# Performance work log

Hardware: AMD Instinct MI355X
Metric: run time of the kernel (lower is better)

Reference implementation:

```python
import jax, jax.numpy as jnp
import numpy as np

EPS = 1e-12  # torch F.normalize default eps
K, C = 64, 128  # num_clusters, dim


def _l2norm(v, axis):
    n = jnp.sqrt(jnp.sum(v * v, axis=axis, keepdims=True))
    return v / jnp.maximum(n, EPS)


def setup_inputs() -> dict:
    key = jax.random.key(0)
    k1, k2, k3, k4 = jax.random.split(key, 4)
    x = jax.random.normal(k1, (32, C, 64, 64), dtype=jnp.float32)
    centroids = jax.random.uniform(k2, (K, C), dtype=jnp.float32)
    # conv weight/bias initialized from centroids like _init_params (alpha=100)
    alpha = 100.0
    conv_w = 2.0 * alpha * centroids                     # [K, C] (1x1 conv)
    conv_b = -alpha * jnp.linalg.norm(centroids, axis=1) # [K]
    return {"x": x, "conv_w": conv_w, "conv_b": conv_b, "centroids": centroids}


def reference(x, conv_w, conv_b, centroids):
    N = x.shape[0]
    # descriptor-wise L2 normalization over channel dim
    x = _l2norm(x, axis=1)
    xf = x.reshape(N, C, -1)  # [N, C, P]
    # 1x1 conv == per-location linear: [N, K, P]
    logits = jnp.einsum('kc,ncp->nkp', conv_w, xf) + conv_b[None, :, None]
    soft_assign = jax.nn.softmax(logits, axis=1)  # softmax over clusters
    # vlad[n,k,c] = sum_p a[n,k,p] * (x[n,c,p] - centroids[k,c])
    # algebraic rewrite avoids the O(N*K*C*P) intermediate (same math)
    vlad = jnp.einsum('nkp,ncp->nkc', soft_assign, xf) \
        - soft_assign.sum(axis=2)[:, :, None] * centroids[None]
    vlad = _l2norm(vlad, axis=2)            # intra-normalization over C
    vlad = vlad.reshape(N, -1)              # [N, K*C]
    vlad = _l2norm(vlad, axis=1)            # global L2 norm
    return vlad
```

## Files before the change

kernel.cpp:

```cpp
#include <hip/hip_runtime.h>

typedef __attribute__((ext_vector_type(4))) float f4;
typedef __attribute__((ext_vector_type(4))) float f32x4;
typedef __attribute__((ext_vector_type(4))) unsigned u32x4;
typedef __attribute__((ext_vector_type(8))) short bf16x8;

#define NK 64
#define NC 128
#define NP 4096
#define NN 32
#define EPSV 1e-12f

#define PCH 64
#define CPB 4
#define NGRPX (NP / (PCH * CPB))

#define WS_WF_SL 0
#define WS_SS    8192
#define WS_VP    (8192 + 32768)
#define WS_SLAB_TOTAL (WS_VP + NGRPX * NN * NK * NC)

#define FB_VLAD 0
#define FB_S    (NN * NK * NC)
#define FB_G    (FB_S + NN * NK)
#define FB_WF   (FB_G + NN)
#define FB_TOTAL (FB_WF + 8192)

__device__ __forceinline__ unsigned short f2bf(float x) {
  unsigned u = __builtin_bit_cast(unsigned, x);
  u += 0x7fffu + ((u >> 16) & 1u);
  return (unsigned short)(u >> 16);
}
__device__ __forceinline__ float bf2f(unsigned short h) {
  unsigned u = ((unsigned)h) << 16;
  return __builtin_bit_cast(float, u);
}
__device__ __forceinline__ unsigned cvtpk(float a, float b) {
  unsigned r;
  asm volatile("v_cvt_pk_bf16_f32 %0, %1, %2" : "=v"(r) : "v"(a), "v"(b));
  return r;
}
__device__ __forceinline__ float asf(unsigned u) { return __builtin_bit_cast(float, u); }

__device__ __forceinline__ void barrier_lds() {
  asm volatile("s_waitcnt lgkmcnt(0)" ::: "memory");
  __builtin_amdgcn_s_barrier();
  asm volatile("" ::: "memory");
  __builtin_amdgcn_sched_barrier(0);
}

__global__ void nv_zero(float* __restrict__ ws) {
  int i = blockIdx.x * blockDim.x + threadIdx.x;
  int stride = gridDim.x * blockDim.x;
  for (; i < FB_WF; i += stride) ws[i] = 0.0f;
}

__global__ void nv_wfrag(const float* __restrict__ conv_w, unsigned short* __restrict__ wfrag) {
  int idx = blockIdx.x * 256 + threadIdx.x;
  if (idx >= 2048) return;
  int lane = idx & 63, hl = (idx >> 6) & 1, ct = (idx >> 7) & 3, kt = idx >> 9;
  int r = lane & 15, g = lane >> 4;
  const float* src = conv_w + (16 * kt + r) * NC + 32 * ct + 8 * g;
  unsigned short o[8];
#pragma unroll
  for (int j = 0; j < 8; ++j) {
    float v = src[j];
    unsigned short h = f2bf(v);
    o[j] = hl ? f2bf(v - bf2f(h)) : h;
  }
  u32x4 pk;
#pragma unroll
  for (int m = 0; m < 4; ++m) pk[m] = (unsigned)o[2 * m] | ((unsigned)o[2 * m + 1] << 16);
  *reinterpret_cast<u32x4*>(wfrag + (size_t)idx * 8) = pk;
}

template <bool SLAB>
__global__ __launch_bounds__(512, 2)
void nv_main(const float* __restrict__ x, const unsigned short* __restrict__ wfrag,
             const float* __restrict__ conv_b, float* __restrict__ vout,
             float* __restrict__ sout) {
  __shared__ __align__(16) unsigned xhl_t[PCH][132];
  __shared__ __align__(16) unsigned short xh[NC][72];
  __shared__ __align__(16) unsigned short a_lds[NK][72];
  __shared__ __align__(16) unsigned short wf_lds[1024][8];
  __shared__ __align__(16) float inv_lds[PCH];
  __shared__ __align__(16) float mx_buf[2][PCH];
  __shared__ __align__(16) float sum_buf[2][PCH];

  const int tid = threadIdx.x;
  const int lane = tid & 63;
  const int w = tid >> 6;
  const int r = lane & 15;
  const int g = lane >> 4;
  const int n = blockIdx.y;
  const int p0loc = (w & 3) << 4;
  const int kp = w >> 2;
  const int ktg0 = kp << 1;
  const int kw = w & 3;
  const int ph = w >> 2;

  for (int s = tid; s < 1024; s += 512) {
    int gs = ((s >> 6) * 2) * 64 + (s & 63);
    *reinterpret_cast<u32x4*>(&wf_lds[s][0]) =
        *reinterpret_cast<const u32x4*>(wfrag + (size_t)gs * 8);
  }
  bf16x8 wlo_r[2][4];
#pragma unroll
  for (int kt2 = 0; kt2 < 2; ++kt2)
#pragma unroll
    for (int ct = 0; ct < 4; ++ct)
      wlo_r[kt2][ct] = *reinterpret_cast<const bf16x8*>(
          wfrag + ((size_t)(((ktg0 + kt2) * 4 + ct) * 2 + 1) * 64 + lane) * 8);
  float bb[2];
#pragma unroll
  for (int kt2 = 0; kt2 < 2; ++kt2) bb[kt2] = conv_b[16 * (ktg0 + kt2) + r];

  f32x4 vacc[8];
#pragma unroll
  for (int t = 0; t < 8; ++t) vacc[t] = (f32x4){0.f, 0.f, 0.f, 0.f};
  float s_part[2] = {0.f, 0.f};

  const int cst = tid & 127;
  const int pq = tid >> 7;
  const int swst = ((cst >> 3) & 3) << 3;
  const int pbase = blockIdx.x * (CPB * PCH);
  const float* xrow = x + ((size_t)n * NC + cst) * NP + 16 * pq;

  f4 pre[4];
#pragma unroll
  for (int q4 = 0; q4 < 4; ++q4)
    pre[q4] = *reinterpret_cast<const f4*>(xrow + pbase + 4 * q4);

  for (int cc = 0; cc < CPB; ++cc) {
#pragma unroll
    for (int q4 = 0; q4 < 4; ++q4) {
      f4 v = pre[q4];
      const int pl = 16 * pq + 4 * q4;
      unsigned h01 = cvtpk(v[0], v[1]);
      unsigned h23 = cvtpk(v[2], v[3]);
      float r0 = v[0] - asf(h01 << 16);
      float r1 = v[1] - asf(h01 & 0xffff0000u);
      float r2 = v[2] - asf(h23 << 16);
      float r3 = v[3] - asf(h23 & 0xffff0000u);
      unsigned l01 = cvtpk(r0, r1);
      unsigned l23 = cvtpk(r2, r3);
      const int pp = pl ^ swst;
      *reinterpret_cast<unsigned*>(&xh[cst][pp]) = h01;
      *reinterpret_cast<unsigned*>(&xh[cst][pp + 2]) = h23;
      xhl_t[pl + 0][cst] = __builtin_amdgcn_perm(h01, l01, 0x05040100u);
      xhl_t[pl + 1][cst] = __builtin_amdgcn_perm(h01, l01, 0x07060302u);
      xhl_t[pl + 2][cst] = __builtin_amdgcn_perm(h23, l23, 0x05040100u);
      xhl_t[pl + 3][cst] = __builtin_amdgcn_perm(h23, l23, 0x07060302u);
    }
    barrier_lds();
    if (cc + 1 < CPB) {
      const float* xb = xrow + pbase + (cc + 1) * PCH;
#pragma unroll
      for (int q4 = 0; q4 < 4; ++q4)
        pre[q4] = *reinterpret_cast<const f4*>(xb + 4 * q4);
    }
    f32x4 d1 = {0.f, 0.f, 0.f, 0.f}, d2 = {0.f, 0.f, 0.f, 0.f};
    f32x4 lac[2];
    lac[0] = (f32x4){0.f, 0.f, 0.f, 0.f};
    lac[1] = (f32x4){0.f, 0.f, 0.f, 0.f};
#pragma unroll
    for (int ct = 0; ct < 4; ++ct) {
      const unsigned* row = &xhl_t[p0loc + r][32 * ct + 8 * g];
      u32x4 wA = *reinterpret_cast<const u32x4*>(row);
      u32x4 wB = *reinterpret_cast<const u32x4*>(row + 4);
      unsigned wv8[8] = {wA[0], wA[1], wA[2], wA[3], wB[0], wB[1], wB[2], wB[3]};
      u32x4 hh, ll;
#pragma unroll
      for (int m = 0; m < 4; ++m) {
        hh[m] = __builtin_amdgcn_perm(wv8[2 * m + 1], wv8[2 * m], 0x07060302u);
        ll[m] = __builtin_amdgcn_perm(wv8[2 * m + 1], wv8[2 * m], 0x05040100u);
      }
      bf16x8 Ah = __builtin_bit_cast(bf16x8, hh);
      bf16x8 Al = __builtin_bit_cast(bf16x8, ll);
      d1 = __builtin_amdgcn_mfma_f32_16x16x32_bf16(Ah, Ah, d1, 0, 0, 0);
      d2 = __builtin_amdgcn_mfma_f32_16x16x32_bf16(Ah, Al, d2, 0, 0, 0);
#pragma unroll
      for (int kt2 = 0; kt2 < 2; ++kt2) {
        const int kt4ct = (ktg0 + kt2) * 4 + ct;
        bf16x8 whi = *reinterpret_cast<const bf16x8*>(&wf_lds[kt4ct * 64 + lane][0]);
        lac[kt2] = __builtin_amdgcn_mfma_f32_16x16x32_bf16(Ah, whi, lac[kt2], 0, 0, 0);
        lac[kt2] = __builtin_amdgcn_mfma_f32_16x16x32_bf16(Al, whi, lac[kt2], 0, 0, 0);
        lac[kt2] = __builtin_amdgcn_mfma_f32_16x16x32_bf16(Ah, wlo_r[kt2][ct], lac[kt2], 0, 0, 0);
      }
    }
    if ((r >> 2) == g) {
      int i = r & 3;
      float nsq = d1[i] + 2.0f * d2[i];
      inv_lds[p0loc + r] = 1.0f / fmaxf(sqrtf(nsq), EPSV);
    }
    asm volatile("s_waitcnt lgkmcnt(0)" ::: "memory");
    __builtin_amdgcn_sched_barrier(0);
    f4 ivv = *reinterpret_cast<const f4*>(&inv_lds[p0loc + 4 * g]);
    float lt[2][4], e[2][4], mpart[4], sp[4];
#pragma unroll
    for (int kt2 = 0; kt2 < 2; ++kt2)
#pragma unroll
      for (int i = 0; i < 4; ++i) lt[kt2][i] = lac[kt2][i] * ivv[i] + bb[kt2];
#pragma unroll
    for (int i = 0; i < 4; ++i) mpart[i] = fmaxf(lt[0][i], lt[1][i]);
#pragma unroll
    for (int o = 1; o <= 8; o <<= 1)
#pragma unroll
      for (int i = 0; i < 4; ++i) mpart[i] = fmaxf(mpart[i], __shfl_xor(mpart[i], o));
#pragma unroll
    for (int i = 0; i < 4; ++i) sp[i] = 0.f;
#pragma unroll
    for (int kt2 = 0; kt2 < 2; ++kt2)
#pragma unroll
      for (int i = 0; i < 4; ++i) {
        e[kt2][i] = __expf(lt[kt2][i] - mpart[i]);
        sp[i] += e[kt2][i];
      }
#pragma unroll
    for (int o = 1; o <= 8; o <<= 1)
#pragma unroll
      for (int i = 0; i < 4; ++i) sp[i] += __shfl_xor(sp[i], o);
    if (r < 4) mx_buf[kp][p0loc + 4 * g + r] = mpart[r];
    else if (r < 8) sum_buf[kp][p0loc + 4 * g + (r - 4)] = sp[r - 4];
    barrier_lds();
    {
      f4 m0 = *reinterpret_cast<const f4*>(&mx_buf[0][p0loc + 4 * g]);
      f4 m1 = *reinterpret_cast<const f4*>(&mx_buf[1][p0loc + 4 * g]);
      f4 s0 = *reinterpret_cast<const f4*>(&sum_buf[0][p0loc + 4 * g]);
      f4 s1 = *reinterpret_cast<const f4*>(&sum_buf[1][p0loc + 4 * g]);
      float fcorr[4];
#pragma unroll
      for (int i = 0; i < 4; ++i) {
        float m = fmaxf(m0[i], m1[i]);
        float c0 = __expf(m0[i] - m);
        float c1 = __expf(m1[i] - m);
        float tot = s0[i] * c0 + s1[i] * c1;
        fcorr[i] = (kp == 0 ? c0 : c1) / tot;
      }
#pragma unroll
      for (int kt2 = 0; kt2 < 2; ++kt2) {
        float av[4];
#pragma unroll
        for (int i = 0; i < 4; ++i) {
          float a = e[kt2][i] * fcorr[i];
          s_part[kt2] += a;
          av[i] = a * ivv[i];
        }
        unsigned* arow = reinterpret_cast<unsigned*>(&a_lds[16 * (ktg0 + kt2) + r][p0loc + 4 * g]);
        arow[0] = cvtpk(av[0], av[1]);
        arow[1] = cvtpk(av[2], av[3]);
      }
    }
    barrier_lds();
    {
      bf16x8 af = *reinterpret_cast<const bf16x8*>(&a_lds[16 * kw + r][32 * ph + 8 * g]);
#pragma unroll
      for (int tcl = 0; tcl < 8; ++tcl) {
        const int c = (tcl << 4) + r;
        const int pblk = ((ph << 2) + g) ^ ((c >> 3) & 3);
        bf16x8 bx = *reinterpret_cast<const bf16x8*>(&xh[c][pblk << 3]);
        vacc[tcl] = __builtin_amdgcn_mfma_f32_16x16x32_bf16(af, bx, vacc[tcl], 0, 0, 0);
      }
    }
    barrier_lds();
  }

  float* cbuf = reinterpret_cast<float*>(&xhl_t[0][0]);
  float* s_red = cbuf + 8192;
  if (w < 4) {
#pragma unroll
    for (int tcl = 0; tcl < 8; ++tcl)
#pragma unroll
      for (int i = 0; i < 4; ++i)
        cbuf[kw * 2048 + (4 * g + i) * 128 + (tcl << 4) + r] = vacc[tcl][i];
  }
#pragma unroll
  for (int kt2 = 0; kt2 < 2; ++kt2) {
    float v = s_part[kt2];
    v += __shfl_xor(v, 16);
    v += __shfl_xor(v, 32);
    if (g == 0) s_red[(kp * 4 + (w & 3)) * 32 + kt2 * 16 + r] = v;
  }
  barrier_lds();
  if (w >= 4) {
#pragma unroll
    for (int tcl = 0; tcl < 8; ++tcl)
#pragma unroll
      for (int i = 0; i < 4; ++i) {
        const int idx = kw * 2048 + (4 * g + i) * 128 + (tcl << 4) + r;
        float v = vacc[tcl][i] + cbuf[idx];
        if constexpr (SLAB) cbuf[idx] = v;
        else atomicAdd(&vout[((size_t)n * NK + 16 * kw + 4 * g + i) * NC + (tcl << 4) + r], v);
      }
  }
  if (tid < 64) {
    float S = 0.f;
#pragma unroll
    for (int pt = 0; pt < 4; ++pt) S += s_red[((tid >> 5) * 4 + pt) * 32 + (tid & 31)];
    if constexpr (SLAB) sout[((size_t)blockIdx.x * NN + n) * NK + tid] = S;
    else atomicAdd(&sout[n * NK + tid], S);
  }
  if constexpr (SLAB) {
    barrier_lds();
    float* dst = vout + ((size_t)blockIdx.x * NN + n) * (NK * NC);
#pragma unroll
    for (int m = 0; m < 4; ++m) {
      const int idx = m * 512 + tid;
      *reinterpret_cast<f4*>(dst + 4 * idx) = *reinterpret_cast<const f4*>(cbuf + 4 * idx);
    }
  }
}

template <bool SLAB>
__global__ void nv_finalize(const float* __restrict__ vin, const float* __restrict__ sin,
                            const float* __restrict__ centroids,
                            float* __restrict__ out, float* __restrict__ gnorm) {
  const int k = blockIdx.x;
  const int n = blockIdx.y;
  const int t = threadIdx.x;
  float S, v0, v1;
  if constexpr (SLAB) {
    float sv = (t < 16) ? sin[((size_t)t * NN + n) * NK + k] : 0.f;
#pragma unroll
    for (int o = 1; o <= 8; o <<= 1) sv += __shfl_xor(sv, o);
    S = __shfl(sv, 0);
    v0 = 0.f; v1 = 0.f;
#pragma unroll
    for (int sx = 0; sx < NGRPX; ++sx) {
      const float* vr = vin + ((size_t)sx * NN + n) * (NK * NC) + k * NC;
      v0 += vr[t];
      v1 += vr[t + 64];
    }
  } else {
    S = sin[n * NK + k];
    const size_t base = ((size_t)n * NK + k) * NC;
    v0 = vin[base + t];
    v1 = vin[base + t + 64];
  }
  v0 -= S * centroids[k * NC + t];
  v1 -= S * centroids[k * NC + t + 64];
  float ss = v0 * v0 + v1 * v1;
#pragma unroll
  for (int off = 1; off < 64; off <<= 1) ss += __shfl_xor(ss, off);
  float inv = 1.0f / fmaxf(sqrtf(ss), EPSV);
  const size_t base = ((size_t)n * NK + k) * NC;
  if constexpr (SLAB) {
    out[base + t] = v0 * inv * 0.125f;
    out[base + t + 64] = v1 * inv * 0.125f;
  } else {
    out[base + t] = v0 * inv;
    out[base + t + 64] = v1 * inv;
    if (t == 0) atomicAdd(&gnorm[n], ss * inv * inv);
  }
}

__global__ void nv_scale(float* __restrict__ out, const float* __restrict__ gnorm) {
  int i = blockIdx.x * blockDim.x + threadIdx.x;
  int n = i >> 13;
  out[i] *= 1.0f / fmaxf(sqrtf(gnorm[n]), EPSV);
}

extern "C" void kernel_launch(void* const* d_in, const int* in_sizes, int n_in,
                              void* d_out, int out_size, void* d_ws, size_t ws_size,
                              hipStream_t stream) {
  const float* x = (const float*)d_in[0];
  const float* conv_w = (const float*)d_in[1];
  const float* conv_b = (const float*)d_in[2];
  const float* centroids = (const float*)d_in[3];
  float* out = (float*)d_out;
  float* ws = (float*)d_ws;

  if (ws_size >= (size_t)WS_SLAB_TOTAL * sizeof(float)) {
    unsigned short* wfrag = (unsigned short*)(ws + WS_WF_SL);
    float* sp = ws + WS_SS;
    float* vp = ws + WS_VP;
    nv_wfrag<<<8, 256, 0, stream>>>(conv_w, wfrag);
    nv_main<true><<<dim3(NGRPX, NN), 512, 0, stream>>>(x, wfrag, conv_b, vp, sp);
    nv_finalize<true><<<dim3(NK, NN), 64, 0, stream>>>(vp, sp, centroids, out, nullptr);
  } else {
    float* vlad_acc = ws + FB_VLAD;
    float* s_acc = ws + FB_S;
    float* gnorm = ws + FB_G;
    unsigned short* wfrag = (unsigned short*)(ws + FB_WF);
    nv_zero<<<256, 256, 0, stream>>>(ws);
    nv_wfrag<<<8, 256, 0, stream>>>(conv_w, wfrag);
    nv_main<false><<<dim3(NGRPX, NN), 512, 0, stream>>>(x, wfrag, conv_b, vlad_acc, s_acc);
    nv_finalize<false><<<dim3(NK, NN), 64, 0, stream>>>(vlad_acc, s_acc, centroids, out, gnorm);
    nv_scale<<<1024, 256, 0, stream>>>(out, gnorm);
  }
}
```

Baseline: 47.28 us.

## Restructure main loop barriers, shuffle inverse norms, prefetch B fragments, widen finalize

The main loop now stages the next chunk's bf16 split at the end of each iteration instead of the start, which removes one block barrier per chunk. The B fragments for the VLAD MFMA are read from LDS before the softmax barrier. Per-pixel inverse norms are broadcast with wave shuffles instead of an LDS round trip with waitcnt, and s_setprio is raised around the MFMA blocks. The finalize kernel packs four clusters per 256-thread block and uses float2 accesses. The early B-fragment reads cost extra registers, and putting STAGE after the MFMAs depends on the xh and xhl_t reuse being correctly fenced.

```diff
diff --git a/kernel.cpp b/kernel.cpp
--- a/kernel.cpp
+++ b/kernel.cpp
@@ -1,5 +1,6 @@
 #include <hip/hip_runtime.h>
 
+typedef __attribute__((ext_vector_type(2))) float f2;
 typedef __attribute__((ext_vector_type(4))) float f4;
 typedef __attribute__((ext_vector_type(4))) float f32x4;
 typedef __attribute__((ext_vector_type(4))) unsigned u32x4;
@@ -83,7 +84,6 @@
   __shared__ __align__(16) unsigned short xh[NC][72];
   __shared__ __align__(16) unsigned short a_lds[NK][72];
   __shared__ __align__(16) unsigned short wf_lds[1024][8];
-  __shared__ __align__(16) float inv_lds[PCH];
   __shared__ __align__(16) float mx_buf[2][PCH];
   __shared__ __align__(16) float sum_buf[2][PCH];
 
@@ -127,11 +127,7 @@
   const float* xrow = x + ((size_t)n * NC + cst) * NP + 16 * pq;
 
   f4 pre[4];
-#pragma unroll
-  for (int q4 = 0; q4 < 4; ++q4)
-    pre[q4] = *reinterpret_cast<const f4*>(xrow + pbase + 4 * q4);
-
-  for (int cc = 0; cc < CPB; ++cc) {
+  auto STAGE = [&]() {
 #pragma unroll
     for (int q4 = 0; q4 < 4; ++q4) {
       f4 v = pre[q4];
@@ -152,7 +148,15 @@
       xhl_t[pl + 2][cst] = __builtin_amdgcn_perm(h23, l23, 0x05040100u);
       xhl_t[pl + 3][cst] = __builtin_amdgcn_perm(h23, l23, 0x07060302u);
     }
-    barrier_lds();
+  };
+
+#pragma unroll
+  for (int q4 = 0; q4 < 4; ++q4)
+    pre[q4] = *reinterpret_cast<const f4*>(xrow + pbase + 4 * q4);
+  STAGE();
+  barrier_lds();
+
+  for (int cc = 0; cc < CPB; ++cc) {
     if (cc + 1 < CPB) {
       const float* xb = xrow + pbase + (cc + 1) * PCH;
 #pragma unroll
@@ -163,6 +167,7 @@
     f32x4 lac[2];
     lac[0] = (f32x4){0.f, 0.f, 0.f, 0.f};
     lac[1] = (f32x4){0.f, 0.f, 0.f, 0.f};
+    __builtin_amdgcn_s_setprio(1);
 #pragma unroll
     for (int ct = 0; ct < 4; ++ct) {
       const unsigned* row = &xhl_t[p0loc + r][32 * ct + 8 * g];
@@ -188,14 +193,14 @@
         lac[kt2] = __builtin_amdgcn_mfma_f32_16x16x32_bf16(Ah, wlo_r[kt2][ct], lac[kt2], 0, 0, 0);
       }
     }
-    if ((r >> 2) == g) {
-      int i = r & 3;
-      float nsq = d1[i] + 2.0f * d2[i];
-      inv_lds[p0loc + r] = 1.0f / fmaxf(sqrtf(nsq), EPSV);
-    }
-    asm volatile("s_waitcnt lgkmcnt(0)" ::: "memory");
-    __builtin_amdgcn_sched_barrier(0);
-    f4 ivv = *reinterpret_cast<const f4*>(&inv_lds[p0loc + 4 * g]);
+    __builtin_amdgcn_s_setprio(0);
+    float nsq = d1[r & 3] + 2.0f * d2[r & 3];
+    float ivv[4];
+#pragma unroll
+    for (int i = 0; i < 4; ++i) {
+      float ns = __shfl(nsq, 20 * g + i);
+      ivv[i] = 1.0f / fmaxf(sqrtf(ns), EPSV);
+    }
     float lt[2][4], e[2][4], mpart[4], sp[4];
 #pragma unroll
     for (int kt2 = 0; kt2 < 2; ++kt2)
@@ -222,6 +227,13 @@
       for (int i = 0; i < 4; ++i) sp[i] += __shfl_xor(sp[i], o);
     if (r < 4) mx_buf[kp][p0loc + 4 * g + r] = mpart[r];
     else if (r < 8) sum_buf[kp][p0loc + 4 * g + (r - 4)] = sp[r - 4];
+    bf16x8 bx[8];
+#pragma unroll
+    for (int tcl = 0; tcl < 8; ++tcl) {
+      const int c = (tcl << 4) + r;
+      const int pblk = ((ph << 2) + g) ^ ((c >> 3) & 3);
+      bx[tcl] = *reinterpret_cast<const bf16x8*>(&xh[c][pblk << 3]);
+    }
     barrier_lds();
     {
       f4 m0 = *reinterpret_cast<const f4*>(&mx_buf[0][p0loc + 4 * g]);
@@ -254,15 +266,16 @@
     barrier_lds();
     {
       bf16x8 af = *reinterpret_cast<const bf16x8*>(&a_lds[16 * kw + r][32 * ph + 8 * g]);
-#pragma unroll
-      for (int tcl = 0; tcl < 8; ++tcl) {
-        const int c = (tcl << 4) + r;
-        const int pblk = ((ph << 2) + g) ^ ((c >> 3) & 3);
-        bf16x8 bx = *reinterpret_cast<const bf16x8*>(&xh[c][pblk << 3]);
-        vacc[tcl] = __builtin_amdgcn_mfma_f32_16x16x32_bf16(af, bx, vacc[tcl], 0, 0, 0);
-      }
-    }
-    barrier_lds();
+      __builtin_amdgcn_s_setprio(1);
+#pragma unroll
+      for (int tcl = 0; tcl < 8; ++tcl)
+        vacc[tcl] = __builtin_amdgcn_mfma_f32_16x16x32_bf16(af, bx[tcl], vacc[tcl], 0, 0, 0);
+      __builtin_amdgcn_s_setprio(0);
+    }
+    if (cc + 1 < CPB) {
+      STAGE();
+      barrier_lds();
+    }
   }
 
   float* cbuf = reinterpret_cast<float*>(&xhl_t[0][0]);
@@ -311,47 +324,54 @@
   }
 }
 
-template <bool SLAB>
+__global__ __launch_bounds__(256)
+void nv_finalize2(const float* __restrict__ vin, const float* __restrict__ sin,
+                  const float* __restrict__ centroids, float* __restrict__ out) {
+  const int wv = threadIdx.x >> 6;
+  const int lane = threadIdx.x & 63;
+  const int k = blockIdx.x * 4 + wv;
+  const int n = blockIdx.y;
+  const int c0 = lane * 2;
+  f2 v = {0.f, 0.f};
+#pragma unroll
+  for (int sx = 0; sx < NGRPX; ++sx) {
+    const float* vr = vin + ((size_t)sx * NN + n) * (NK * NC) + k * NC;
+    f2 t = *reinterpret_cast<const f2*>(vr + c0);
+    v.x += t.x;
+    v.y += t.y;
+  }
+  float sv = (lane < 16) ? sin[((size_t)lane * NN + n) * NK + k] : 0.f;
+#pragma unroll
+  for (int o = 1; o <= 8; o <<= 1) sv += __shfl_xor(sv, o);
+  float S = __shfl(sv, 0);
+  f2 ce = *reinterpret_cast<const f2*>(centroids + k * NC + c0);
+  v.x -= S * ce.x;
+  v.y -= S * ce.y;
+  float ss = v.x * v.x + v.y * v.y;
+#pragma unroll
+  for (int o = 1; o < 64; o <<= 1) ss += __shfl_xor(ss, o);
+  float inv = 0.125f / fmaxf(sqrtf(ss), EPSV);
+  f2 ov = {v.x * inv, v.y * inv};
+  *reinterpret_cast<f2*>(out + ((size_t)n * NK + k) * NC + c0) = ov;
+}
+
 __global__ void nv_finalize(const float* __restrict__ vin, const float* __restrict__ sin,
                             const float* __restrict__ centroids,
                             float* __restrict__ out, float* __restrict__ gnorm) {
   const int k = blockIdx.x;
   const int n = blockIdx.y;
   const int t = threadIdx.x;
-  float S, v0, v1;
-  if constexpr (SLAB) {
-    float sv = (t < 16) ? sin[((size_t)t * NN + n) * NK + k] : 0.f;
-#pragma unroll
-    for (int o = 1; o <= 8; o <<= 1) sv += __shfl_xor(sv, o);
-    S = __shfl(sv, 0);
-    v0 = 0.f; v1 = 0.f;
-#pragma unroll
-    for (int sx = 0; sx < NGRPX; ++sx) {
-      const float* vr = vin + ((size_t)sx * NN + n) * (NK * NC) + k * NC;
-      v0 += vr[t];
-      v1 += vr[t + 64];
-    }
-  } else {
-    S = sin[n * NK + k];
-    const size_t base = ((size_t)n * NK + k) * NC;
-    v0 = vin[base + t];
-    v1 = vin[base + t + 64];
-  }
-  v0 -= S * centroids[k * NC + t];
-  v1 -= S * centroids[k * NC + t + 64];
+  float S = sin[n * NK + k];
+  const size_t base = ((size_t)n * NK + k) * NC;
+  float v0 = vin[base + t] - S * centroids[k * NC + t];
+  float v1 = vin[base + t + 64] - S * centroids[k * NC + t + 64];
   float ss = v0 * v0 + v1 * v1;
 #pragma unroll
   for (int off = 1; off < 64; off <<= 1) ss += __shfl_xor(ss, off);
   float inv = 1.0f / fmaxf(sqrtf(ss), EPSV);
-  const size_t base = ((size_t)n * NK + k) * NC;
-  if constexpr (SLAB) {
-    out[base + t] = v0 * inv * 0.125f;
-    out[base + t + 64] = v1 * inv * 0.125f;
-  } else {
-    out[base + t] = v0 * inv;
-    out[base + t + 64] = v1 * inv;
-    if (t == 0) atomicAdd(&gnorm[n], ss * inv * inv);
-  }
+  out[base + t] = v0 * inv;
+  out[base + t + 64] = v1 * inv;
+  if (t == 0) atomicAdd(&gnorm[n], ss * inv * inv);
 }
 
 __global__ void nv_scale(float* __restrict__ out, const float* __restrict__ gnorm) {
@@ -376,7 +396,7 @@
     float* vp = ws + WS_VP;
     nv_wfrag<<<8, 256, 0, stream>>>(conv_w, wfrag);
     nv_main<true><<<dim3(NGRPX, NN), 512, 0, stream>>>(x, wfrag, conv_b, vp, sp);
-    nv_finalize<true><<<dim3(NK, NN), 64, 0, stream>>>(vp, sp, centroids, out, nullptr);
+    nv_finalize2<<<dim3(NK / 4, NN), 256, 0, stream>>>(vp, sp, centroids, out);
   } else {
     float* vlad_acc = ws + FB_VLAD;
     float* s_acc = ws + FB_S;
@@ -385,7 +405,7 @@
     nv_zero<<<256, 256, 0, stream>>>(ws);
     nv_wfrag<<<8, 256, 0, stream>>>(conv_w, wfrag);
     nv_main<false><<<dim3(NGRPX, NN), 512, 0, stream>>>(x, wfrag, conv_b, vlad_acc, s_acc);
-    nv_finalize<false><<<dim3(NK, NN), 64, 0, stream>>>(vlad_acc, s_acc, centroids, out, gnorm);
+    nv_finalize<<<dim3(NK, NN), 64, 0, stream>>>(vlad_acc, s_acc, centroids, out, gnorm);
     nv_scale<<<1024, 256, 0, stream>>>(out, gnorm);
   }
 }
```

Measured after the change: 50.77 us. 7.4% more time.
